# Optimization experiments

Measured on AMD Instinct MI355X. Metric: run time of the kernel, lower is better.

Reference implementation:

```python
import jax, jax.numpy as jnp
import numpy as np

N_NODES = 100000
N_FEAT = 256
HIDDEN = 16
N_CLASSES = 16
N_EDGES = 3200000


def setup_inputs() -> dict:
    key = jax.random.key(0)
    k = jax.random.split(key, 7)
    x = jax.random.normal(k[0], (N_NODES, N_FEAT), dtype=jnp.float32)
    edge_index = jax.random.randint(k[1], (2, N_EDGES), 0, N_NODES, dtype=jnp.int32)
    # GCNConv: linear (no bias) + bias added after aggregation
    s1 = 1.0 / np.sqrt(N_FEAT)
    W1 = jax.random.uniform(k[2], (N_FEAT, HIDDEN), jnp.float32, -s1, s1)
    b1 = jnp.zeros((HIDDEN,), jnp.float32)
    # SAGEConv: lin_l (on aggregated neighbors, with bias) + lin_r (root)
    s2 = 1.0 / np.sqrt(HIDDEN)
    Wl = jax.random.uniform(k[3], (HIDDEN, N_CLASSES), jnp.float32, -s2, s2)
    Wr = jax.random.uniform(k[4], (HIDDEN, N_CLASSES), jnp.float32, -s2, s2)
    b2 = jax.random.uniform(k[5], (N_CLASSES,), jnp.float32, -s2, s2)
    return {"x": x, "edge_index": edge_index, "W1": W1, "b1": b1,
            "Wl": Wl, "Wr": Wr, "b2": b2}


def reference(x, edge_index, W1, b1, Wl, Wr, b2):
    N = x.shape[0]
    src, dst = edge_index[0], edge_index[1]

    # ---- GCNConv(num_features -> hidden): transform, add self-loops,
    # symmetric normalization, sum-aggregate, add bias ----
    h = x @ W1  # [N, H]
    loop = jnp.arange(N, dtype=src.dtype)
    src2 = jnp.concatenate([src, loop])
    dst2 = jnp.concatenate([dst, loop])
    ones = jnp.ones(src2.shape[0], dtype=h.dtype)
    deg = jax.ops.segment_sum(ones, dst2, num_segments=N)  # in-degree incl. self-loop
    dinv = jnp.where(deg > 0, jax.lax.rsqrt(deg), 0.0)
    norm = dinv[src2] * dinv[dst2]  # [E+N]
    msgs = h[src2] * norm[:, None]
    h1 = jax.ops.segment_sum(msgs, dst2, num_segments=N) + b1  # [N, H]

    # ---- SAGEConv(hidden -> num_classes, aggr='mean') ----
    cnt = jax.ops.segment_sum(jnp.ones(src.shape[0], dtype=h1.dtype), dst, num_segments=N)
    agg = jax.ops.segment_sum(h1[src], dst, num_segments=N)
    agg = agg / jnp.maximum(cnt, 1.0)[:, None]  # mean over neighbors
    out = agg @ Wl + h1 @ Wr + b2  # [N, C]

    return jax.nn.log_softmax(out, axis=1)
```

## Files before the change

kernel.cpp:

```cpp
#include <hip/hip_runtime.h>
#include <cstddef>

#define NF 256
#define NH 16
#define NC 16

#define BN    128
#define BSH   7
#define BMSK  127
#define CAP   4608
#define AVLEN 32
#define ACH   (256*AVLEN)
#define NBMAX 800

typedef __attribute__((ext_vector_type(8))) short bf16x8;
typedef __attribute__((ext_vector_type(4))) float f32x4;

__device__ inline short f2bf(float f) {
    union { float f; unsigned int u; } v; v.f = f;
    const unsigned int r = v.u + 0x7FFFu + ((v.u >> 16) & 1u);
    return (short)(r >> 16);
}
__device__ inline float bf2f(unsigned short u) {
    union { unsigned int i; float f; } v; v.i = ((unsigned int)u) << 16;
    return v.f;
}

__global__ __launch_bounds__(256) void bucketA_kernel(
    const int* __restrict__ src, const int* __restrict__ dst,
    unsigned int* __restrict__ bfill, unsigned int* __restrict__ bpairs,
    int E, int NBK)
{
    __shared__ unsigned int hist[NBMAX];
    __shared__ unsigned int sbase[NBMAX];
    __shared__ unsigned int gpos[NBMAX];
    __shared__ unsigned int tmp[1024];
    __shared__ unsigned int reorder[ACH];
    __shared__ unsigned short wbid[ACH];

    const int tid = threadIdx.x;
    for (int i = tid; i < NBMAX; i += 256) hist[i] = 0u;
    __syncthreads();

    const int base = blockIdx.x * ACH;
    unsigned int pv[AVLEN];
    unsigned int ps[AVLEN];
    #pragma unroll
    for (int l = 0; l < AVLEN; ++l) {
        const int e = base + l * 256 + tid;
        if (e < E) {
            const unsigned int s = (unsigned int)src[e];
            const unsigned int d = (unsigned int)dst[e];
            const unsigned int b = d >> BSH;
            pv[l] = (s << BSH) | (d & BMSK);
            const unsigned int slot = atomicAdd(&hist[b], 1u);
            ps[l] = (slot << 10) | b;
        } else {
            ps[l] = 0xFFFFFFFFu;
        }
    }
    __syncthreads();

    for (int i = tid; i < 1024; i += 256) tmp[i] = (i < NBK) ? hist[i] : 0u;
    __syncthreads();
    for (int off = 1; off < 1024; off <<= 1) {
        unsigned int v0 = 0, v1 = 0, v2 = 0, v3 = 0;
        const int i0 = tid, i1 = tid + 256, i2 = tid + 512, i3 = tid + 768;
        if (i0 >= off) v0 = tmp[i0 - off];
        if (i1 >= off) v1 = tmp[i1 - off];
        if (i2 >= off) v2 = tmp[i2 - off];
        if (i3 >= off) v3 = tmp[i3 - off];
        __syncthreads();
        tmp[i0] += v0; tmp[i1] += v1; tmp[i2] += v2; tmp[i3] += v3;
        __syncthreads();
    }
    for (int i = tid; i < NBK; i += 256) {
        const unsigned int h = hist[i];
        sbase[i] = tmp[i] - h;
        if (h) gpos[i] = atomicAdd(&bfill[i], h);
    }
    const int cc = (base + ACH <= E) ? ACH : (E - base);
    __syncthreads();

    #pragma unroll
    for (int l = 0; l < AVLEN; ++l) {
        if (ps[l] != 0xFFFFFFFFu) {
            const unsigned int b = ps[l] & 1023u;
            const unsigned int i = sbase[b] + (ps[l] >> 10);
            reorder[i] = pv[l];
            wbid[i] = (unsigned short)b;
        }
    }
    __syncthreads();

    for (int i = tid; i < cc; i += 256) {
        const unsigned int b = wbid[i];
        const unsigned int g = gpos[b] + ((unsigned int)i - sbase[b]);
        if (g < CAP) bpairs[(size_t)b * CAP + g] = reorder[i];
    }
}

__global__ __launch_bounds__(256) void bucketB_gemm_kernel(
    const unsigned int* __restrict__ bfill, unsigned int* __restrict__ bpairs,
    const float* __restrict__ x, const float* __restrict__ W1,
    int* __restrict__ rowptr, int* __restrict__ cnt, float* __restrict__ dinv,
    unsigned short* __restrict__ hs_bf, int N)
{
    __shared__ unsigned int pairs[CAP];
    __shared__ unsigned int ssorted[CAP];
    __shared__ unsigned int hist[BN];
    __shared__ unsigned int scan[BN];
    __shared__ unsigned int cursor[BN];
    __shared__ float sdinv[BN];

    const int tid = threadIdx.x;
    const int b = blockIdx.x;
    const size_t bbase = (size_t)b * CAP;
    unsigned int m = bfill[b]; if (m > CAP) m = CAP;

    const int lane = threadIdx.x & 63;
    const int wave = threadIdx.x >> 6;
    const int quad = lane >> 4;
    const int mn   = lane & 15;
    bf16x8 bfrag[8];
    #pragma unroll
    for (int kc = 0; kc < 8; ++kc) {
        #pragma unroll
        for (int j = 0; j < 8; ++j) {
            const int k = kc * 32 + quad * 8 + j;
            bfrag[kc][j] = f2bf(W1[k * NH + mn]);
        }
    }

    if (tid < BN) hist[tid] = 0u;
    __syncthreads();

    for (unsigned int i = tid; i < m; i += 256) {
        const unsigned int p = bpairs[bbase + i];
        pairs[i] = p;
        atomicAdd(&hist[p & BMSK], 1u);
    }
    __syncthreads();

    if (tid < BN) scan[tid] = hist[tid];
    __syncthreads();
    for (int off = 1; off < BN; off <<= 1) {
        unsigned int v = 0;
        if (tid < BN && tid >= off) v = scan[tid - off];
        __syncthreads();
        if (tid < BN) scan[tid] += v;
        __syncthreads();
    }
    if (tid < BN) cursor[tid] = scan[tid] - hist[tid];
    __syncthreads();

    for (unsigned int i = tid; i < m; i += 256) {
        const unsigned int p = pairs[i];
        const unsigned int pos = atomicAdd(&cursor[p & BMSK], 1u);
        ssorted[pos] = p >> BSH;
    }
    __syncthreads();

    for (unsigned int i = tid; i < m; i += 256)
        bpairs[bbase + i] = ssorted[i];

    if (tid < BN) {
        const int n = b * BN + tid;
        const unsigned int h = hist[tid];
        const float dv = rsqrtf((float)h + 1.0f);
        sdinv[tid] = dv;
        if (n < N) {
            cnt[n] = (int)h;
            dinv[n] = dv;
            rowptr[n] = (int)(b * CAP + (scan[tid] - h));
        }
    }
    __syncthreads();

    #pragma unroll
    for (int t = 0; t < 2; ++t) {
        const int tile = b * 8 + wave * 2 + t;
        const int n0 = tile * 16;
        if (n0 >= N) break;

        f32x4 acc = {0.f, 0.f, 0.f, 0.f};
        const float* xrow = x + (size_t)(n0 + mn) * NF + quad * 8;
        #pragma unroll
        for (int kc = 0; kc < 8; ++kc) {
            const float4 lo = *(const float4*)(xrow + kc * 32);
            const float4 hi = *(const float4*)(xrow + kc * 32 + 4);
            bf16x8 af;
            af[0] = f2bf(lo.x); af[1] = f2bf(lo.y); af[2] = f2bf(lo.z); af[3] = f2bf(lo.w);
            af[4] = f2bf(hi.x); af[5] = f2bf(hi.y); af[6] = f2bf(hi.z); af[7] = f2bf(hi.w);
            acc = __builtin_amdgcn_mfma_f32_16x16x32_bf16(af, bfrag[kc], acc, 0, 0, 0);
        }

        const int lbase = n0 - b * BN + quad * 4;
        #pragma unroll
        for (int r = 0; r < 4; ++r) {
            const int row = quad * 4 + r;
            hs_bf[(size_t)(n0 + row) * NH + mn] =
                (unsigned short)f2bf(acc[r] * sdinv[lbase + r]);
        }
    }
}

__global__ __launch_bounds__(256) void gcn_gather_kernel(
    const unsigned short* __restrict__ hs_bf, const unsigned int* __restrict__ csrc,
    const int* __restrict__ rowptr, const int* __restrict__ cnt,
    const float* __restrict__ dinv, const float* __restrict__ b1,
    unsigned short* __restrict__ h1_bf, int N)
{
    const int tid = threadIdx.x;
    const int n = blockIdx.x * 16 + (tid >> 4);
    if (n >= N) return;
    const int j = tid & 15;
    const int start = rowptr[n];
    const int end = start + cnt[n];

    float acc = bf2f(hs_bf[(size_t)n * NH + j]);
    int k = start;
    for (; k + 16 <= end; k += 16) {
        const int myi = (int)csrc[k + j];
        float s = 0.f;
        #pragma unroll
        for (int u = 0; u < 16; ++u) {
            const int sidx = __shfl(myi, u, 16);
            s += bf2f(hs_bf[(size_t)sidx * NH + j]);
        }
        acc += s;
    }
    for (; k < end; ++k)
        acc += bf2f(hs_bf[(size_t)csrc[k] * NH + j]);

    h1_bf[(size_t)n * NH + j] = (unsigned short)f2bf(b1[j] + dinv[n] * acc);
}

__global__ __launch_bounds__(256) void sage_out_kernel(
    const unsigned short* __restrict__ h1_bf, const unsigned int* __restrict__ csrc,
    const int* __restrict__ rowptr, const int* __restrict__ cnt,
    const float* __restrict__ Wl, const float* __restrict__ Wr,
    const float* __restrict__ b2, float* __restrict__ out, int N)
{
    __shared__ float wls[NH * NC];
    __shared__ float wrs[NH * NC];
    __shared__ float b2s[NC];
    const int tid = threadIdx.x;
    if (tid < NH * NC) { wls[tid] = Wl[tid]; wrs[tid] = Wr[tid]; }
    if (tid < NC) b2s[tid] = b2[tid];
    __syncthreads();

    const int n = blockIdx.x * 16 + (tid >> 4);
    if (n >= N) return;
    const int j = tid & 15;
    const int start = rowptr[n];
    const int deg = cnt[n];
    const int end = start + deg;

    float acc = 0.f;
    int k = start;
    for (; k + 16 <= end; k += 16) {
        const int myi = (int)csrc[k + j];
        float s = 0.f;
        #pragma unroll
        for (int u = 0; u < 16; ++u) {
            const int sidx = __shfl(myi, u, 16);
            s += bf2f(h1_bf[(size_t)sidx * NH + j]);
        }
        acc += s;
    }
    for (; k < end; ++k)
        acc += bf2f(h1_bf[(size_t)csrc[k] * NH + j]);

    const float aggj = acc / fmaxf((float)deg, 1.0f);
    const float h1j  = bf2f(h1_bf[(size_t)n * NH + j]);

    float o = b2s[j];
    #pragma unroll
    for (int kk = 0; kk < NH; ++kk) {
        const float a  = __shfl(aggj, kk, 16);
        const float hh = __shfl(h1j,  kk, 16);
        o += a * wls[kk * NC + j] + hh * wrs[kk * NC + j];
    }

    float m = o;
    #pragma unroll
    for (int off = 1; off < 16; off <<= 1) m = fmaxf(m, __shfl_xor(m, off, 16));
    const float ex = expf(o - m);
    float ssum = ex;
    #pragma unroll
    for (int off = 1; off < 16; off <<= 1) ssum += __shfl_xor(ssum, off, 16);

    out[(size_t)n * NC + j] = (o - m) - logf(ssum);
}

extern "C" void kernel_launch(void* const* d_in, const int* in_sizes, int n_in,
                              void* d_out, int out_size, void* d_ws, size_t ws_size,
                              hipStream_t stream)
{
    const float* x  = (const float*)d_in[0];
    const int*   ei = (const int*)d_in[1];
    const float* W1 = (const float*)d_in[2];
    const float* b1 = (const float*)d_in[3];
    const float* Wl = (const float*)d_in[4];
    const float* Wr = (const float*)d_in[5];
    const float* b2 = (const float*)d_in[6];
    float* out = (float*)d_out;

    const int N = in_sizes[0] / NF;
    const int E = in_sizes[1] / 2;
    const int* src = ei;
    const int* dst = ei + E;

    const int NBK = (N + BN - 1) / BN;

    unsigned short* hs_bf = (unsigned short*)d_ws;
    unsigned short* h1_bf = hs_bf + (size_t)N * NH;
    float* dinv   = (float*)(h1_bf + (size_t)N * NH);
    int*   cnt    = (int*)(dinv + N);
    int*   rowptr = cnt + N;
    unsigned int* bfill  = (unsigned int*)(rowptr + N);
    unsigned int* bpairs = bfill + 1024;

    hipMemsetAsync(bfill, 0, (size_t)NBK * sizeof(unsigned int), stream);

    bucketA_kernel<<<(E + ACH - 1) / ACH, 256, 0, stream>>>(src, dst, bfill, bpairs, E, NBK);
    bucketB_gemm_kernel<<<NBK, 256, 0, stream>>>(bfill, bpairs, x, W1, rowptr, cnt, dinv, hs_bf, N);

    const int nodeBlk = (N + 15) / 16;
    gcn_gather_kernel<<<nodeBlk, 256, 0, stream>>>(hs_bf, bpairs, rowptr, cnt, dinv, b1, h1_bf, N);
    sage_out_kernel<<<nodeBlk, 256, 0, stream>>>(h1_bf, bpairs, rowptr, cnt, Wl, Wr, b2, out, N);
}
```

Measured before the change: 311.9 us.

## Run X·W1 GEMM concurrently with edge bucketing in one fused launch

```diff
diff --git a/kernel.cpp b/kernel.cpp
--- a/kernel.cpp
+++ b/kernel.cpp
@@ -9,7 +9,7 @@
 #define BSH   7
 #define BMSK  127
 #define CAP   4608
-#define AVLEN 32
+#define AVLEN 16
 #define ACH   (256*AVLEN)
 #define NBMAX 800
 
@@ -26,10 +26,11 @@
     return v.f;
 }
 
-__global__ __launch_bounds__(256) void bucketA_kernel(
+__global__ __launch_bounds__(256) void fusedAG_kernel(
     const int* __restrict__ src, const int* __restrict__ dst,
     unsigned int* __restrict__ bfill, unsigned int* __restrict__ bpairs,
-    int E, int NBK)
+    const float* __restrict__ x, const float* __restrict__ W1,
+    float* __restrict__ hs_u, int E, int NBK, int NCH, int N)
 {
     __shared__ unsigned int hist[NBMAX];
     __shared__ unsigned int sbase[NBMAX];
@@ -39,70 +40,114 @@
     __shared__ unsigned short wbid[ACH];
 
     const int tid = threadIdx.x;
-    for (int i = tid; i < NBMAX; i += 256) hist[i] = 0u;
-    __syncthreads();
-
-    const int base = blockIdx.x * ACH;
-    unsigned int pv[AVLEN];
-    unsigned int ps[AVLEN];
-    #pragma unroll
-    for (int l = 0; l < AVLEN; ++l) {
-        const int e = base + l * 256 + tid;
-        if (e < E) {
-            const unsigned int s = (unsigned int)src[e];
-            const unsigned int d = (unsigned int)dst[e];
-            const unsigned int b = d >> BSH;
-            pv[l] = (s << BSH) | (d & BMSK);
-            const unsigned int slot = atomicAdd(&hist[b], 1u);
-            ps[l] = (slot << 10) | b;
-        } else {
-            ps[l] = 0xFFFFFFFFu;
-        }
-    }
-    __syncthreads();
-
-    for (int i = tid; i < 1024; i += 256) tmp[i] = (i < NBK) ? hist[i] : 0u;
-    __syncthreads();
-    for (int off = 1; off < 1024; off <<= 1) {
-        unsigned int v0 = 0, v1 = 0, v2 = 0, v3 = 0;
-        const int i0 = tid, i1 = tid + 256, i2 = tid + 512, i3 = tid + 768;
-        if (i0 >= off) v0 = tmp[i0 - off];
-        if (i1 >= off) v1 = tmp[i1 - off];
-        if (i2 >= off) v2 = tmp[i2 - off];
-        if (i3 >= off) v3 = tmp[i3 - off];
-        __syncthreads();
-        tmp[i0] += v0; tmp[i1] += v1; tmp[i2] += v2; tmp[i3] += v3;
-        __syncthreads();
-    }
-    for (int i = tid; i < NBK; i += 256) {
-        const unsigned int h = hist[i];
-        sbase[i] = tmp[i] - h;
-        if (h) gpos[i] = atomicAdd(&bfill[i], h);
-    }
-    const int cc = (base + ACH <= E) ? ACH : (E - base);
-    __syncthreads();
-
-    #pragma unroll
-    for (int l = 0; l < AVLEN; ++l) {
-        if (ps[l] != 0xFFFFFFFFu) {
-            const unsigned int b = ps[l] & 1023u;
-            const unsigned int i = sbase[b] + (ps[l] >> 10);
-            reorder[i] = pv[l];
-            wbid[i] = (unsigned short)b;
-        }
-    }
-    __syncthreads();
-
-    for (int i = tid; i < cc; i += 256) {
-        const unsigned int b = wbid[i];
-        const unsigned int g = gpos[b] + ((unsigned int)i - sbase[b]);
-        if (g < CAP) bpairs[(size_t)b * CAP + g] = reorder[i];
-    }
-}
-
-__global__ __launch_bounds__(256) void bucketB_gemm_kernel(
+
+    if (blockIdx.x < (unsigned)NCH) {
+        for (int i = tid; i < NBMAX; i += 256) hist[i] = 0u;
+        __syncthreads();
+
+        const int base = blockIdx.x * ACH;
+        unsigned int pv[AVLEN];
+        unsigned int ps[AVLEN];
+        #pragma unroll
+        for (int l = 0; l < AVLEN; ++l) {
+            const int e = base + l * 256 + tid;
+            if (e < E) {
+                const unsigned int s = (unsigned int)src[e];
+                const unsigned int d = (unsigned int)dst[e];
+                const unsigned int b = d >> BSH;
+                pv[l] = (s << BSH) | (d & BMSK);
+                const unsigned int slot = atomicAdd(&hist[b], 1u);
+                ps[l] = (slot << 10) | b;
+            } else {
+                ps[l] = 0xFFFFFFFFu;
+            }
+        }
+        __syncthreads();
+
+        for (int i = tid; i < 1024; i += 256) tmp[i] = (i < NBK) ? hist[i] : 0u;
+        __syncthreads();
+        for (int off = 1; off < 1024; off <<= 1) {
+            unsigned int v0 = 0, v1 = 0, v2 = 0, v3 = 0;
+            const int i0 = tid, i1 = tid + 256, i2 = tid + 512, i3 = tid + 768;
+            if (i0 >= off) v0 = tmp[i0 - off];
+            if (i1 >= off) v1 = tmp[i1 - off];
+            if (i2 >= off) v2 = tmp[i2 - off];
+            if (i3 >= off) v3 = tmp[i3 - off];
+            __syncthreads();
+            tmp[i0] += v0; tmp[i1] += v1; tmp[i2] += v2; tmp[i3] += v3;
+            __syncthreads();
+        }
+        for (int i = tid; i < NBK; i += 256) {
+            const unsigned int h = hist[i];
+            sbase[i] = tmp[i] - h;
+            if (h) gpos[i] = atomicAdd(&bfill[i], h);
+        }
+        const int cc = (base + ACH <= E) ? ACH : (E - base);
+        __syncthreads();
+
+        #pragma unroll
+        for (int l = 0; l < AVLEN; ++l) {
+            if (ps[l] != 0xFFFFFFFFu) {
+                const unsigned int b = ps[l] & 1023u;
+                const unsigned int i = sbase[b] + (ps[l] >> 10);
+                reorder[i] = pv[l];
+                wbid[i] = (unsigned short)b;
+            }
+        }
+        __syncthreads();
+
+        for (int i = tid; i < cc; i += 256) {
+            const unsigned int b = wbid[i];
+            const unsigned int g = gpos[b] + ((unsigned int)i - sbase[b]);
+            if (g < CAP) bpairs[(size_t)b * CAP + g] = reorder[i];
+        }
+    } else {
+        const int gb = blockIdx.x - NCH;
+        const int lane = tid & 63;
+        const int wave = tid >> 6;
+        const int quad = lane >> 4;
+        const int mn   = lane & 15;
+
+        bf16x8 bfrag[8];
+        #pragma unroll
+        for (int kc = 0; kc < 8; ++kc) {
+            #pragma unroll
+            for (int j = 0; j < 8; ++j) {
+                const int k = kc * 32 + quad * 8 + j;
+                bfrag[kc][j] = f2bf(W1[k * NH + mn]);
+            }
+        }
+
+        #pragma unroll
+        for (int t = 0; t < 2; ++t) {
+            const int tile = gb * 8 + wave * 2 + t;
+            const int n0 = tile * 16;
+            if (n0 >= N) break;
+
+            f32x4 acc = {0.f, 0.f, 0.f, 0.f};
+            const float* xrow = x + (size_t)(n0 + mn) * NF + quad * 8;
+            #pragma unroll
+            for (int kc = 0; kc < 8; ++kc) {
+                const float4 lo = *(const float4*)(xrow + kc * 32);
+                const float4 hi = *(const float4*)(xrow + kc * 32 + 4);
+                bf16x8 af;
+                af[0] = f2bf(lo.x); af[1] = f2bf(lo.y); af[2] = f2bf(lo.z); af[3] = f2bf(lo.w);
+                af[4] = f2bf(hi.x); af[5] = f2bf(hi.y); af[6] = f2bf(hi.z); af[7] = f2bf(hi.w);
+                acc = __builtin_amdgcn_mfma_f32_16x16x32_bf16(af, bfrag[kc], acc, 0, 0, 0);
+            }
+
+            #pragma unroll
+            for (int r = 0; r < 4; ++r) {
+                const int row = quad * 4 + r;
+                hs_u[(size_t)(n0 + row) * NH + mn] = acc[r];
+            }
+        }
+    }
+}
+
+__global__ __launch_bounds__(256) void bucketB_kernel(
     const unsigned int* __restrict__ bfill, unsigned int* __restrict__ bpairs,
-    const float* __restrict__ x, const float* __restrict__ W1,
+    const float* __restrict__ hs_u,
     int* __restrict__ rowptr, int* __restrict__ cnt, float* __restrict__ dinv,
     unsigned short* __restrict__ hs_bf, int N)
 {
@@ -116,21 +161,8 @@
     const int tid = threadIdx.x;
     const int b = blockIdx.x;
     const size_t bbase = (size_t)b * CAP;
+    const int nodeBase = b * BN;
     unsigned int m = bfill[b]; if (m > CAP) m = CAP;
-
-    const int lane = threadIdx.x & 63;
-    const int wave = threadIdx.x >> 6;
-    const int quad = lane >> 4;
-    const int mn   = lane & 15;
-    bf16x8 bfrag[8];
-    #pragma unroll
-    for (int kc = 0; kc < 8; ++kc) {
-        #pragma unroll
-        for (int j = 0; j < 8; ++j) {
-            const int k = kc * 32 + quad * 8 + j;
-            bfrag[kc][j] = f2bf(W1[k * NH + mn]);
-        }
-    }
 
     if (tid < BN) hist[tid] = 0u;
     __syncthreads();
@@ -165,7 +197,7 @@
         bpairs[bbase + i] = ssorted[i];
 
     if (tid < BN) {
-        const int n = b * BN + tid;
+        const int n = nodeBase + tid;
         const unsigned int h = hist[tid];
         const float dv = rsqrtf((float)h + 1.0f);
         sdinv[tid] = dv;
@@ -177,30 +209,11 @@
     }
     __syncthreads();
 
-    #pragma unroll
-    for (int t = 0; t < 2; ++t) {
-        const int tile = b * 8 + wave * 2 + t;
-        const int n0 = tile * 16;
-        if (n0 >= N) break;
-
-        f32x4 acc = {0.f, 0.f, 0.f, 0.f};
-        const float* xrow = x + (size_t)(n0 + mn) * NF + quad * 8;
-        #pragma unroll
-        for (int kc = 0; kc < 8; ++kc) {
-            const float4 lo = *(const float4*)(xrow + kc * 32);
-            const float4 hi = *(const float4*)(xrow + kc * 32 + 4);
-            bf16x8 af;
-            af[0] = f2bf(lo.x); af[1] = f2bf(lo.y); af[2] = f2bf(lo.z); af[3] = f2bf(lo.w);
-            af[4] = f2bf(hi.x); af[5] = f2bf(hi.y); af[6] = f2bf(hi.z); af[7] = f2bf(hi.w);
-            acc = __builtin_amdgcn_mfma_f32_16x16x32_bf16(af, bfrag[kc], acc, 0, 0, 0);
-        }
-
-        const int lbase = n0 - b * BN + quad * 4;
-        #pragma unroll
-        for (int r = 0; r < 4; ++r) {
-            const int row = quad * 4 + r;
-            hs_bf[(size_t)(n0 + row) * NH + mn] =
-                (unsigned short)f2bf(acc[r] * sdinv[lbase + r]);
+    for (int t = tid; t < BN * NH; t += 256) {
+        const int n = nodeBase + (t >> 4);
+        if (n < N) {
+            const size_t idx = (size_t)n * NH + (t & 15);
+            hs_bf[idx] = (unsigned short)f2bf(hs_u[idx] * sdinv[t >> 4]);
         }
     }
 }
@@ -313,10 +326,14 @@
     const int* dst = ei + E;
 
     const int NBK = (N + BN - 1) / BN;
+    const int NCH = (E + ACH - 1) / ACH;
+    const int tiles = (N + 15) / 16;
+    const int GEMMB = (tiles + 7) / 8;
 
     unsigned short* hs_bf = (unsigned short*)d_ws;
     unsigned short* h1_bf = hs_bf + (size_t)N * NH;
-    float* dinv   = (float*)(h1_bf + (size_t)N * NH);
+    float* hs_u   = (float*)(h1_bf + (size_t)N * NH);
+    float* dinv   = hs_u + (size_t)N * NH;
     int*   cnt    = (int*)(dinv + N);
     int*   rowptr = cnt + N;
     unsigned int* bfill  = (unsigned int*)(rowptr + N);
@@ -324,8 +341,10 @@
 
     hipMemsetAsync(bfill, 0, (size_t)NBK * sizeof(unsigned int), stream);
 
-    bucketA_kernel<<<(E + ACH - 1) / ACH, 256, 0, stream>>>(src, dst, bfill, bpairs, E, NBK);
-    bucketB_gemm_kernel<<<NBK, 256, 0, stream>>>(bfill, bpairs, x, W1, rowptr, cnt, dinv, hs_bf, N);
+    fusedAG_kernel<<<NCH + GEMMB, 256, 0, stream>>>(
+        src, dst, bfill, bpairs, x, W1, hs_u, E, NBK, NCH, N);
+    bucketB_kernel<<<NBK, 256, 0, stream>>>(
+        bfill, bpairs, hs_u, rowptr, cnt, dinv, hs_bf, N);
 
     const int nodeBlk = (N + 15) / 16;
     gcn_gather_kernel<<<nodeBlk, 256, 0, stream>>>(hs_bf, bpairs, rowptr, cnt, dinv, b1, h1_bf, N);
```

Result: no change. 316.0 us (+1.3%).
